# Kernel tuning notes

Hardware: AMD Instinct MI355X
Metric: run time of the kernel (lower is better)

Reference implementation:

```python
import jax, jax.numpy as jnp
import numpy as np

D = 1024        # model dim (== moe_inter_dim, required by Expert's x2*x3)
H = 1024        # expert hidden dim (moe_inter_dim)
E = 8           # n_routed_experts
K = 2           # n_activated_experts (top-k)
I = 2 * 1024    # shared-expert inter dim = n_shared_experts * moe_inter_dim
ROUTE_SCALE = 1.0


def setup_inputs() -> dict:
    key = jax.random.key(0)
    ks = jax.random.split(key, 12)
    s = lambda *sh: 1.0 / np.sqrt(sh[-1])
    return {
        "x":      jax.random.normal(ks[0], (1, 2048, D), jnp.float32),
        "gate_w": jax.random.normal(ks[1], (E, D), jnp.float32) * s(E, D),
        "w1":     jax.random.normal(ks[2], (E, H, D), jnp.float32) * s(H, D),
        "b1":     jax.random.normal(ks[3], (E, H), jnp.float32) * 0.01,
        "w2":     jax.random.normal(ks[4], (E, D, H), jnp.float32) * s(D, H),
        "b2":     jax.random.normal(ks[5], (E, D), jnp.float32) * 0.01,
        "w3":     jax.random.normal(ks[6], (E, H, D), jnp.float32) * s(H, D),
        "b3":     jax.random.normal(ks[7], (E, H), jnp.float32) * 0.01,
        "sw1":    jax.random.normal(ks[8], (I, D), jnp.float32) * s(I, D),
        "sw2":    jax.random.normal(ks[9], (I, D), jnp.float32) * s(I, D),
        "sw3":    jax.random.normal(ks[10], (D, I), jnp.float32) * s(D, I),
    }


def reference(x, gate_w, w1, b1, w2, b2, w3, b3, sw1, sw2, sw3):
    B, S, _ = x.shape
    xt = x.reshape(-1, D)                                  # (T, D)
    # ---- Gate (softmax scoring, n_groups==1, no bias, route_scale=1) ----
    logits = xt @ gate_w.T                                 # (T, E)
    scores = jax.nn.softmax(logits.astype(jnp.float32), axis=-1)
    top_vals, idx = jax.lax.top_k(scores, K)               # (T, K)
    weights = (jnp.take_along_axis(scores, idx, axis=1)
               .astype(x.dtype)) * ROUTE_SCALE             # (T, K)
    # ---- Routed experts: input is scaled by routing weight BEFORE expert ----
    xs = xt[:, None, :] * weights[:, :, None]              # (T, K, D)
    y = jnp.zeros_like(xt)
    for e in range(E):  # fixed small loop over experts (dense masked dispatch)
        mask = (idx == e).astype(x.dtype)                  # (T, K)
        h = jax.nn.silu(jnp.einsum('tkd,hd->tkh', xs, w1[e]) + b1[e])
        x2 = jnp.einsum('tkh,dh->tkd', h, w2[e]) + b2[e]   # (T, K, D)
        x3 = jnp.einsum('tkd,hd->tkh', xs, w3[e]) + b3[e]  # (T, K, H==D)
        y = y + jnp.sum((x2 * x3) * mask[:, :, None], axis=1)
    # ---- Shared experts (SwiGLU MLP, no biases) ----
    z = (jax.nn.silu(xt @ sw1.T) * (xt @ sw2.T)) @ sw3.T   # (T, D)
    return (y + z).reshape(B, S, D)
```

## Files before the change

### kernel.cpp

```cpp
#include <hip/hip_runtime.h>

typedef unsigned short u16;
typedef __attribute__((ext_vector_type(4))) float floatx4;
typedef __attribute__((ext_vector_type(8))) short short8;

#define MAXROWS 5120

__device__ __forceinline__ u16 f2bf(float f) {
    union { float f; unsigned u; } v; v.f = f;
    unsigned r = v.u + 0x7FFF + ((v.u >> 16) & 1);
    return (u16)(r >> 16);
}
__device__ __forceinline__ float bf2f(u16 h) {
    union { unsigned u; float f; } v; v.u = ((unsigned)h) << 16; return v.f;
}
__device__ __forceinline__ float silu_f(float x) { return x / (1.f + __expf(-x)); }

__device__ __forceinline__ void gl_lds16(const void* g, void* l) {
    __builtin_amdgcn_global_load_lds(
        (__attribute__((address_space(1))) unsigned int*)g,
        (__attribute__((address_space(3))) unsigned int*)l, 16, 0, 0);
}

__device__ __forceinline__ void ld_frags(
    unsigned a0, unsigned a1, unsigned a2, unsigned a3,
    unsigned b0, unsigned b1, unsigned b2, unsigned b3,
    short8& af0, short8& af1, short8& af2, short8& af3,
    short8& bf0, short8& bf1, short8& bf2, short8& bf3) {
    asm volatile(
        "ds_read_b128 %0, %8\n\t"
        "ds_read_b128 %1, %9\n\t"
        "ds_read_b128 %2, %10\n\t"
        "ds_read_b128 %3, %11\n\t"
        "ds_read_b128 %4, %12\n\t"
        "ds_read_b128 %5, %13\n\t"
        "ds_read_b128 %6, %14\n\t"
        "ds_read_b128 %7, %15\n\t"
        "s_waitcnt lgkmcnt(0)"
        : "=&v"(af0), "=&v"(af1), "=&v"(af2), "=&v"(af3),
          "=&v"(bf0), "=&v"(bf1), "=&v"(bf2), "=&v"(bf3)
        : "v"(a0), "v"(a1), "v"(a2), "v"(a3),
          "v"(b0), "v"(b1), "v"(b2), "v"(b3));
}

__device__ __forceinline__ void ld_frags4(
    unsigned a0, unsigned a1, unsigned a2, unsigned a3,
    short8& f0, short8& f1, short8& f2, short8& f3) {
    asm volatile(
        "ds_read_b128 %0, %4\n\t"
        "ds_read_b128 %1, %5\n\t"
        "ds_read_b128 %2, %6\n\t"
        "ds_read_b128 %3, %7\n\t"
        "s_waitcnt lgkmcnt(0)"
        : "=&v"(f0), "=&v"(f1), "=&v"(f2), "=&v"(f3)
        : "v"(a0), "v"(a1), "v"(a2), "v"(a3));
}

#define WAIT_VM8() __builtin_amdgcn_s_waitcnt(3960)
#define WAIT_VM4() __builtin_amdgcn_s_waitcnt(3956)
#define WAIT_VM0() __builtin_amdgcn_s_waitcnt(3952)
#define BAR()      __builtin_amdgcn_s_barrier()

__global__ void conv_gate(const float* __restrict__ w1, const float* __restrict__ w2,
                          const float* __restrict__ w3, const float* __restrict__ sw1,
                          const float* __restrict__ sw2, const float* __restrict__ sw3,
                          const float* __restrict__ x, const float* __restrict__ gw,
                          u16* __restrict__ W13, u16* __restrict__ W2b,
                          u16* __restrict__ S12, u16* __restrict__ S3b,
                          u16* __restrict__ Xb,
                          int* __restrict__ idxA, float* __restrict__ wA) {
    int bid = blockIdx.x;
    if (bid < 512) {
        int w = threadIdx.x >> 6, lane = threadIdx.x & 63;
        int t = bid * 4 + w;
        const float* xr = x + (size_t)t * 1024;
        float acc[8];
#pragma unroll
        for (int e = 0; e < 8; e++) acc[e] = 0.f;
#pragma unroll
        for (int i = 0; i < 16; i++) {
            float xv = xr[lane + (i << 6)];
#pragma unroll
            for (int e = 0; e < 8; e++) acc[e] += xv * gw[e * 1024 + lane + (i << 6)];
        }
#pragma unroll
        for (int e = 0; e < 8; e++)
            for (int off = 32; off > 0; off >>= 1) acc[e] += __shfl_xor(acc[e], off);
        if (lane == 0) {
            float m = acc[0];
#pragma unroll
            for (int e = 1; e < 8; e++) m = fmaxf(m, acc[e]);
            float p[8], s = 0.f;
#pragma unroll
            for (int e = 0; e < 8; e++) { p[e] = __expf(acc[e] - m); s += p[e]; }
            float inv = 1.f / s;
#pragma unroll
            for (int e = 0; e < 8; e++) p[e] *= inv;
            int i0 = 0;
#pragma unroll
            for (int e = 1; e < 8; e++) if (p[e] > p[i0]) i0 = e;
            int i1 = (i0 == 0) ? 1 : 0;
            for (int e = i1 + 1; e < 8; e++) if (e != i0 && p[e] > p[i1]) i1 = e;
            idxA[2 * t] = i0; idxA[2 * t + 1] = i1;
            wA[2 * t] = p[i0]; wA[2 * t + 1] = p[i1];
        }
        return;
    }
    long j = (long)(bid - 512) * 256 + threadIdx.x;
    const float* src; u16* dst; long d;
    if (j < 2097152) {
        long e = j >> 18; src = w1; dst = W13; d = j + (e << 18);
    } else if ((j -= 2097152) < 2097152) {
        long e = j >> 18; src = w3; dst = W13; d = j + (e << 18) + 262144;
    } else if ((j -= 2097152) < 2097152) { src = w2;  dst = W2b; d = j; }
    else if ((j -= 2097152) < 524288) {
        long rr = j >> 8, c4 = j & 255;
        long br = ((rr >> 4) << 5) + (rr & 15);
        src = sw1; dst = S12; d = (br << 8) + c4;
    } else if ((j -= 524288) < 524288) {
        long rr = j >> 8, c4 = j & 255;
        long br = ((rr >> 4) << 5) + 16 + (rr & 15);
        src = sw2; dst = S12; d = (br << 8) + c4;
    } else if ((j -= 524288) < 524288)     { src = sw3; dst = S3b; d = j; }
    else { j -= 524288; src = x; dst = Xb; d = j; }
    float4 v = ((const float4*)src)[j];
    ushort4 o; o.x = f2bf(v.x); o.y = f2bf(v.y); o.z = f2bf(v.z); o.w = f2bf(v.w);
    ((ushort4*)dst)[d] = o;
}

__global__ void rank_k(const int* __restrict__ idxA, int* __restrict__ tileexp,
                       int* __restrict__ tilem0, int* __restrict__ tilevalid,
                       int* __restrict__ ntiles, int* __restrict__ slot_of) {
    int lane = threadIdx.x;
    const int* my = idxA + lane * 64;
    int h[8];
#pragma unroll
    for (int e = 0; e < 8; e++) h[e] = 0;
    for (int i = 0; i < 64; i++) {
        int v = my[i];
#pragma unroll
        for (int e = 0; e < 8; e++) h[e] += (v == e);
    }
    int excl[8], tot[8];
#pragma unroll
    for (int e = 0; e < 8; e++) {
        int inc = h[e];
        for (int off = 1; off < 64; off <<= 1) {
            int up = __shfl_up(inc, off);
            if (lane >= off) inc += up;
        }
        excl[e] = inc - h[e];
        tot[e] = __shfl(inc, 63);
    }
    int base[8], tiles = 0;
#pragma unroll
    for (int e = 0; e < 8; e++) {
        base[e] = tiles * 128;
        tiles += (tot[e] + 127) >> 7;
    }
    if (lane == 0) {
        int t256 = 0;
        for (int e = 0; e < 8; e++) {
            int t128 = (tot[e] + 127) >> 7;
            for (int j = 0; j < t128; j += 2) {
                tileexp[t256] = e;
                tilem0[t256] = base[e] + (j << 7);
                tilevalid[t256] = ((t128 - j) >= 2) ? 256 : 128;
                t256++;
            }
        }
        ntiles[0] = t256;
    }
    int c[8];
#pragma unroll
    for (int e = 0; e < 8; e++) c[e] = base[e] + excl[e];
    for (int i = 0; i < 64; i++) {
        int v = my[i], slot = 0;
#pragma unroll
        for (int e = 0; e < 8; e++) slot += (v == e) ? c[e] : 0;
#pragma unroll
        for (int e = 0; e < 8; e++) c[e] += (v == e);
        slot_of[lane * 64 + i] = slot;
    }
}

__global__ void build_xs(const float* __restrict__ x, const float* __restrict__ wA,
                         const int* __restrict__ slot_of, u16* __restrict__ XS) {
    int s = blockIdx.x, i = threadIdx.x;
    int t = s >> 1; float w = wA[s]; int slot = slot_of[s];
    float4 v = ((const float4*)(x + (size_t)t * 1024))[i];
    ushort4 o; o.x = f2bf(v.x * w); o.y = f2bf(v.y * w); o.z = f2bf(v.z * w); o.w = f2bf(v.w * w);
    ((ushort4*)(XS + (size_t)slot * 1024))[i] = o;
}

#define STAGE_PAIR(Ab, Bb, lda, kbeg, TT, RND)                                 \
    {                                                                          \
        int r_ = (w << 4) + ((RND) << 7) + rloc;                               \
        int cg_ = clds ^ ((r_ >> 1) & 3);                                      \
        int kk_ = (kbeg) + ((TT) << 5);                                        \
        int db_ = (((TT) & 3) << 14) + (((w << 4) + ((RND) << 7)) << 5);       \
        gl_lds16((Ab) + (size_t)(m0 + r_) * (lda) + kk_ + (cg_ << 3),          \
                 LDS + db_);                                                   \
        gl_lds16((Bb) + (size_t)(n0 + r_) * (lda) + kk_ + (cg_ << 3),          \
                 LDS + 8192 + db_);                                            \
    }

#define MFMA4(AF, IOFF)                                                        \
    _Pragma("unroll")                                                          \
    for (int i_ = 0; i_ < 4; i_++)                                             \
        _Pragma("unroll")                                                      \
        for (int j_ = 0; j_ < 4; j_++)                                         \
            acc[i_ + (IOFF)][j_] = __builtin_amdgcn_mfma_f32_16x16x32_bf16(    \
                AF[i_], bf[j_], acc[i_ + (IOFF)][j_], 0, 0, 0);

#define KLOOP(NSTEP, Ab, Bb, lda, kbeg)                                        \
    {                                                                          \
        STAGE_PAIR(Ab, Bb, lda, kbeg, 0, 0); STAGE_PAIR(Ab, Bb, lda, kbeg, 0, 1); \
        STAGE_PAIR(Ab, Bb, lda, kbeg, 1, 0); STAGE_PAIR(Ab, Bb, lda, kbeg, 1, 1); \
        STAGE_PAIR(Ab, Bb, lda, kbeg, 2, 0); STAGE_PAIR(Ab, Bb, lda, kbeg, 2, 1); \
        WAIT_VM8(); BAR();                                                     \
        for (int t = 0; t < (NSTEP); t++) {                                    \
            unsigned bo = (unsigned)(t & 3) << 15;                             \
            bool more = (t + 3 < (NSTEP));                                     \
            if (more) STAGE_PAIR(Ab, Bb, lda, kbeg, t + 3, 0);                 \
            short8 af[4], bf[4], a2[4];                                        \
            ld_frags(adA[0] + bo, adA[1] + bo, adA[2] + bo, adA[3] + bo,       \
                     adB[0] + bo, adB[1] + bo, adB[2] + bo, adB[3] + bo,       \
                     af[0], af[1], af[2], af[3], bf[0], bf[1], bf[2], bf[3]);  \
            __builtin_amdgcn_s_setprio(1);                                     \
            MFMA4(af, 0);                                                      \
            __builtin_amdgcn_s_setprio(0);                                     \
            if (more) STAGE_PAIR(Ab, Bb, lda, kbeg, t + 3, 1);                 \
            ld_frags4(adA[4] + bo, adA[5] + bo, adA[6] + bo, adA[7] + bo,      \
                      a2[0], a2[1], a2[2], a2[3]);                             \
            if (t < (NSTEP) - 1) {                                             \
                int rem = (NSTEP) - 1 - t;                                     \
                if (rem >= 3) WAIT_VM8();                                      \
                else if (rem == 2) WAIT_VM4();                                 \
                else WAIT_VM0();                                               \
                BAR();                                                         \
            }                                                                  \
            __builtin_amdgcn_s_setprio(1);                                     \
            MFMA4(a2, 4);                                                      \
            __builtin_amdgcn_s_setprio(0);                                     \
        }                                                                      \
    }

#define GEMM_PRE()                                                             \
    int tid = threadIdx.x, w = tid >> 6, lane = tid & 63;                      \
    int wm = w >> 2, wn = w & 3;                                               \
    int rloc = lane >> 2, clds = lane & 3, q = lane >> 4, l15 = lane & 15;     \
    unsigned ldsbase = (unsigned)(size_t)(__attribute__((address_space(3))) u16*)LDS; \
    unsigned adA[8], adB[4];                                                   \
    _Pragma("unroll")                                                          \
    for (int i = 0; i < 8; i++) {                                              \
        int rr = (wm << 7) + (i << 4) + l15;                                   \
        int g = q ^ ((rr >> 1) & 3);                                           \
        adA[i] = ldsbase + rr * 64 + g * 16;                                   \
    }                                                                          \
    _Pragma("unroll")                                                          \
    for (int j = 0; j < 4; j++) {                                              \
        int rr = (wn << 6) + (j << 4) + l15;                                   \
        int g = q ^ ((rr >> 1) & 3);                                           \
        adB[j] = ldsbase + 16384 + rr * 64 + g * 16;                           \
    }                                                                          \
    floatx4 acc[8][4];                                                         \
    _Pragma("unroll")                                                          \
    for (int i = 0; i < 8; i++)                                                \
        _Pragma("unroll")                                                      \
        for (int j = 0; j < 4; j++) {                                          \
            floatx4 z = {0.f, 0.f, 0.f, 0.f}; acc[i][j] = z;                   \
        }

__global__ __launch_bounds__(512, 2) void gemm_A(
    const u16* __restrict__ XS, const u16* __restrict__ Xb,
    const u16* __restrict__ W13, const u16* __restrict__ S12,
    const float* __restrict__ b1, const float* __restrict__ b3,
    u16* __restrict__ H, u16* __restrict__ X3h, u16* __restrict__ G,
    const int* __restrict__ tileexp, const int* __restrict__ tilem0,
    const int* __restrict__ tilevalid, const int* __restrict__ ntiles) {
    __shared__ u16 LDS[65536];
    int xcd = blockIdx.x & 7, ws = blockIdx.x >> 3;
    const u16 *Ab, *Bb; int m0, n0, nt = 0, e = 0, vcnt = 256; bool routed;
    if (ws < 24) {
        routed = true;
        int mt = xcd * 3 + (ws >> 3);
        nt = ws & 7;
        if (mt >= ntiles[0]) return;
        e = tileexp[mt]; m0 = tilem0[mt]; vcnt = tilevalid[mt];
        n0 = nt * 256;
        Ab = XS; Bb = W13 + ((size_t)e << 21);
    } else {
        routed = false; int s = ws - 24;
        m0 = xcd * 256; n0 = s * 256;
        Ab = Xb; Bb = S12;
    }
    GEMM_PRE();

    KLOOP(32, Ab, Bb, 1024, 0);

    if (routed) {
#pragma unroll
        for (int i = 0; i < 8; i++) {
            if (((wm << 7) + (i << 4)) >= vcnt) continue;
            int rowb = m0 + (wm << 7) + (i << 4) + (q << 2);
#pragma unroll
            for (int j = 0; j < 4; j++) {
                int col = n0 + (wn << 6) + (j << 4) + l15;
#pragma unroll
                for (int r = 0; r < 4; r++) {
                    float v = acc[i][j][r];
                    int rw = rowb + r;
                    if (nt < 4) {
                        H[(size_t)rw * 1024 + col] = f2bf(silu_f(v + b1[e * 1024 + col]));
                    } else {
                        int c2 = col - 1024;
                        X3h[(size_t)rw * 1024 + c2] = f2bf(v + b3[e * 1024 + c2]);
                    }
                }
            }
        }
    } else {
#pragma unroll
        for (int i = 0; i < 8; i++) {
            int rowb = m0 + (wm << 7) + (i << 4) + (q << 2);
#pragma unroll
            for (int jp = 0; jp < 4; jp += 2) {
                int brb = n0 + (wn << 6) + (jp << 4);
                int lcol = ((brb >> 5) << 4) + l15;
#pragma unroll
                for (int r = 0; r < 4; r++) {
                    float u = acc[i][jp][r], v = acc[i][jp + 1][r];
                    G[(size_t)(rowb + r) * 2048 + lcol] = f2bf(silu_f(u) * v);
                }
            }
        }
    }
}

__global__ __launch_bounds__(512, 2) void gemm_B(
    const u16* __restrict__ H, const u16* __restrict__ G,
    const u16* __restrict__ W2b, const u16* __restrict__ S3b,
    const float* __restrict__ b2, const u16* __restrict__ X3h,
    u16* __restrict__ P0, u16* __restrict__ P1, float* __restrict__ Z,
    const int* __restrict__ tileexp, const int* __restrict__ tilem0,
    const int* __restrict__ tilevalid, const int* __restrict__ ntiles) {
    __shared__ u16 LDS[65536];
    int xcd = blockIdx.x & 7, ws = blockIdx.x >> 3;
    const u16 *Ab, *Bb; int m0, n0, kc, kbeg, lda, e = 0, vcnt = 256; bool routed;
    if (ws < 24) {
        routed = true;
        int mt = xcd * 3 + (ws >> 3);
        int r = ws & 7; int nt = r & 3; kc = r >> 2;
        if (mt >= ntiles[0]) return;
        e = tileexp[mt]; m0 = tilem0[mt]; vcnt = tilevalid[mt];
        n0 = nt * 256;
        Ab = H; Bb = W2b + ((size_t)e << 20); lda = 1024; kbeg = kc << 9;
    } else {
        routed = false; int s = ws - 24;
        kc = s >> 2; int nt = s & 3;
        m0 = xcd * 256; n0 = nt * 256;
        Ab = G; Bb = S3b; lda = 2048; kbeg = kc << 9;
    }
    GEMM_PRE();

    KLOOP(16, Ab, Bb, lda, kbeg);

    if (routed) {
        u16* Pk = kc ? P1 : P0;
#pragma unroll
        for (int i = 0; i < 8; i++) {
            if (((wm << 7) + (i << 4)) >= vcnt) continue;
            int rowb = m0 + (wm << 7) + (i << 4) + (q << 2);
#pragma unroll
            for (int j = 0; j < 4; j++) {
                int col = n0 + (wn << 6) + (j << 4) + l15;
#pragma unroll
                for (int r = 0; r < 4; r++) {
                    int rw = rowb + r;
                    float v = acc[i][j][r] + (kc == 0 ? b2[e * 1024 + col] : 0.f);
                    float pv = v * bf2f(X3h[(size_t)rw * 1024 + col]);
                    Pk[(size_t)rw * 1024 + col] = f2bf(pv);
                }
            }
        }
    } else {
        float* Zk = Z + (size_t)kc * 2097152;
#pragma unroll
        for (int i = 0; i < 8; i++) {
            int rowb = m0 + (wm << 7) + (i << 4) + (q << 2);
#pragma unroll
            for (int j = 0; j < 4; j++) {
                int col = n0 + (wn << 6) + (j << 4) + l15;
#pragma unroll
                for (int r = 0; r < 4; r++)
                    Zk[(size_t)(rowb + r) * 1024 + col] = acc[i][j][r];
            }
        }
    }
}

__global__ void final_k(const float* __restrict__ Z,
                        const u16* __restrict__ P0, const u16* __restrict__ P1,
                        const int* __restrict__ slot_of, float* __restrict__ out) {
    int i = blockIdx.x * 256 + threadIdx.x;
    int t = i >> 8, c4 = i & 255;
    int s0 = slot_of[2 * t], s1 = slot_of[2 * t + 1];
    size_t zi = (size_t)t * 256 + c4;
    float4 z0 = ((const float4*)Z)[zi];
    float4 z1 = ((const float4*)(Z + 2097152))[zi];
    float4 z2 = ((const float4*)(Z + 4194304))[zi];
    float4 z3 = ((const float4*)(Z + 6291456))[zi];
    ushort4 a0 = ((const ushort4*)P0)[(size_t)s0 * 256 + c4];
    ushort4 a1 = ((const ushort4*)P1)[(size_t)s0 * 256 + c4];
    ushort4 c0 = ((const ushort4*)P0)[(size_t)s1 * 256 + c4];
    ushort4 c1 = ((const ushort4*)P1)[(size_t)s1 * 256 + c4];
    float4 o;
    o.x = z0.x + z1.x + z2.x + z3.x + bf2f(a0.x) + bf2f(a1.x) + bf2f(c0.x) + bf2f(c1.x);
    o.y = z0.y + z1.y + z2.y + z3.y + bf2f(a0.y) + bf2f(a1.y) + bf2f(c0.y) + bf2f(c1.y);
    o.z = z0.z + z1.z + z2.z + z3.z + bf2f(a0.z) + bf2f(a1.z) + bf2f(c0.z) + bf2f(c1.z);
    o.w = z0.w + z1.w + z2.w + z3.w + bf2f(a0.w) + bf2f(a1.w) + bf2f(c0.w) + bf2f(c1.w);
    ((float4*)out)[(size_t)t * 256 + c4] = o;
}

extern "C" void kernel_launch(void* const* d_in, const int* in_sizes, int n_in,
                              void* d_out, int out_size, void* d_ws, size_t ws_size,
                              hipStream_t stream) {
    const float* x   = (const float*)d_in[0];
    const float* gw  = (const float*)d_in[1];
    const float* w1  = (const float*)d_in[2];
    const float* b1  = (const float*)d_in[3];
    const float* w2  = (const float*)d_in[4];
    const float* b2  = (const float*)d_in[5];
    const float* w3  = (const float*)d_in[6];
    const float* b3  = (const float*)d_in[7];
    const float* sw1 = (const float*)d_in[8];
    const float* sw2 = (const float*)d_in[9];
    const float* sw3 = (const float*)d_in[10];
    float* out = (float*)d_out;

    char* p = (char*)d_ws;
    int* ntiles    = (int*)(p + 192);
    int* tileexp   = (int*)(p + 256);
    int* tilem0    = (int*)(p + 512);
    int* tilevalid = (int*)(p + 768);
    size_t off = 4096;
    u16*   XS      = (u16*)(p + off);   off += (size_t)MAXROWS * 1024 * 2;
    int*   idxA    = (int*)(p + off);   off += 16384;
    float* wA      = (float*)(p + off); off += 16384;
    int*   slot_of = (int*)(p + off);   off += 16384;
    u16*   H       = (u16*)(p + off);   off += (size_t)MAXROWS * 1024 * 2;
    u16*   X3h     = (u16*)(p + off);   off += (size_t)MAXROWS * 1024 * 2;
    u16*   P0      = (u16*)(p + off);   off += (size_t)MAXROWS * 1024 * 2;
    u16*   P1      = (u16*)(p + off);   off += (size_t)MAXROWS * 1024 * 2;
    float* Z       = (float*)(p + off); off += (size_t)4 * 2048 * 1024 * 4;
    u16*   W13     = (u16*)(p + off);   off += (size_t)8 * 2048 * 1024 * 2;
    u16*   W2b     = (u16*)(p + off);   off += (size_t)8 * 1024 * 1024 * 2;
    u16*   S12     = (u16*)(p + off);   off += (size_t)4096 * 1024 * 2;
    u16*   S3b     = (u16*)(p + off);   off += (size_t)1024 * 2048 * 2;
    u16*   Xb      = (u16*)(p + off);   off += (size_t)2048 * 1024 * 2;
    u16*   G       = (u16*)(p + off);   off += (size_t)2048 * 2048 * 2;

    conv_gate<<<33280, 256, 0, stream>>>(w1, w2, w3, sw1, sw2, sw3, x, gw,
                                         W13, W2b, S12, S3b, Xb, idxA, wA);
    rank_k<<<1, 64, 0, stream>>>(idxA, tileexp, tilem0, tilevalid, ntiles, slot_of);
    build_xs<<<4096, 256, 0, stream>>>(x, wA, slot_of, XS);

    gemm_A<<<320, 512, 0, stream>>>(XS, Xb, W13, S12, b1, b3, H, X3h, G,
                                    tileexp, tilem0, tilevalid, ntiles);
    gemm_B<<<320, 512, 0, stream>>>(H, G, W2b, S3b, b2, X3h, P0, P1, Z,
                                    tileexp, tilem0, tilevalid, ntiles);
    final_k<<<2048, 256, 0, stream>>>(Z, P0, P1, slot_of, out);
}
```

Baseline: 309.0 us.

## Software-pipeline LDS fragment loads across k-steps with double-buffered registers

Restructures the GEMM k-loop so the next step's A/B fragments are read from LDS while the current step's MFMAs run. It uses two register sets of fragments, partial lgkmcnt waits, and sched_barriers to keep the compiler from reordering. Launch bounds drop from 2 to 1 waves-per-EU target so the extra live fragment registers fit without spilling. The cost is lower occupancy and more register pressure, and the hand-tuned wait counts add risk of subtle hazards.

```diff
diff --git a/kernel.cpp b/kernel.cpp
--- a/kernel.cpp
+++ b/kernel.cpp
@@ -22,11 +22,25 @@
         (__attribute__((address_space(3))) unsigned int*)l, 16, 0, 0);
 }
 
-__device__ __forceinline__ void ld_frags(
+__device__ __forceinline__ void ds4_waitold(
+    unsigned a0, unsigned a1, unsigned a2, unsigned a3,
+    short8& o0, short8& o1, short8& o2, short8& o3) {
+    asm volatile(
+        "ds_read_b128 %0, %4\n\t"
+        "ds_read_b128 %1, %5\n\t"
+        "ds_read_b128 %2, %6\n\t"
+        "ds_read_b128 %3, %7\n\t"
+        "s_waitcnt lgkmcnt(4)"
+        : "=&v"(o0), "=&v"(o1), "=&v"(o2), "=&v"(o3)
+        : "v"(a0), "v"(a1), "v"(a2), "v"(a3));
+    __builtin_amdgcn_sched_barrier(0);
+}
+
+__device__ __forceinline__ void ds8_waitold(
     unsigned a0, unsigned a1, unsigned a2, unsigned a3,
     unsigned b0, unsigned b1, unsigned b2, unsigned b3,
-    short8& af0, short8& af1, short8& af2, short8& af3,
-    short8& bf0, short8& bf1, short8& bf2, short8& bf3) {
+    short8& o0, short8& o1, short8& o2, short8& o3,
+    short8& o4, short8& o5, short8& o6, short8& o7) {
     asm volatile(
         "ds_read_b128 %0, %8\n\t"
         "ds_read_b128 %1, %9\n\t"
@@ -36,27 +50,16 @@
         "ds_read_b128 %5, %13\n\t"
         "ds_read_b128 %6, %14\n\t"
         "ds_read_b128 %7, %15\n\t"
-        "s_waitcnt lgkmcnt(0)"
-        : "=&v"(af0), "=&v"(af1), "=&v"(af2), "=&v"(af3),
-          "=&v"(bf0), "=&v"(bf1), "=&v"(bf2), "=&v"(bf3)
+        "s_waitcnt lgkmcnt(8)"
+        : "=&v"(o0), "=&v"(o1), "=&v"(o2), "=&v"(o3),
+          "=&v"(o4), "=&v"(o5), "=&v"(o6), "=&v"(o7)
         : "v"(a0), "v"(a1), "v"(a2), "v"(a3),
           "v"(b0), "v"(b1), "v"(b2), "v"(b3));
-}
-
-__device__ __forceinline__ void ld_frags4(
-    unsigned a0, unsigned a1, unsigned a2, unsigned a3,
-    short8& f0, short8& f1, short8& f2, short8& f3) {
-    asm volatile(
-        "ds_read_b128 %0, %4\n\t"
-        "ds_read_b128 %1, %5\n\t"
-        "ds_read_b128 %2, %6\n\t"
-        "ds_read_b128 %3, %7\n\t"
-        "s_waitcnt lgkmcnt(0)"
-        : "=&v"(f0), "=&v"(f1), "=&v"(f2), "=&v"(f3)
-        : "v"(a0), "v"(a1), "v"(a2), "v"(a3));
+    __builtin_amdgcn_sched_barrier(0);
 }
 
 #define WAIT_VM8() __builtin_amdgcn_s_waitcnt(3960)
+#define WAIT_VM6() __builtin_amdgcn_s_waitcnt(3958)
 #define WAIT_VM4() __builtin_amdgcn_s_waitcnt(3956)
 #define WAIT_VM0() __builtin_amdgcn_s_waitcnt(3952)
 #define BAR()      __builtin_amdgcn_s_barrier()
@@ -205,13 +208,44 @@
                  LDS + 8192 + db_);                                            \
     }
 
-#define MFMA4(AF, IOFF)                                                        \
+#define MFMA16(AF, BF, IOFF)                                                   \
+    __builtin_amdgcn_s_setprio(1);                                             \
     _Pragma("unroll")                                                          \
     for (int i_ = 0; i_ < 4; i_++)                                             \
         _Pragma("unroll")                                                      \
         for (int j_ = 0; j_ < 4; j_++)                                         \
             acc[i_ + (IOFF)][j_] = __builtin_amdgcn_mfma_f32_16x16x32_bf16(    \
-                AF[i_], bf[j_], acc[i_ + (IOFF)][j_], 0, 0, 0);
+                (AF)[i_], (BF)[j_], acc[i_ + (IOFF)][j_], 0, 0, 0);            \
+    __builtin_amdgcn_s_setprio(0);                                             \
+    __builtin_amdgcn_sched_barrier(0);
+
+#define KSTEP(T, LOc, Fc, LOn, Fn, NSTEP, Ab, Bb, lda, kbeg)                   \
+    {                                                                          \
+        unsigned bo_ = (unsigned)((T) & 3) << 15;                              \
+        if ((T) + 3 < (NSTEP)) STAGE_PAIR(Ab, Bb, lda, kbeg, (T) + 3, 0);      \
+        short8 ah[4];                                                          \
+        ds4_waitold(adA[4] + bo_, adA[5] + bo_, adA[6] + bo_, adA[7] + bo_,    \
+                    ah[0], ah[1], ah[2], ah[3]);                               \
+        BAR();                                                                 \
+        MFMA16(LOc, Fc, 0);                                                    \
+        if ((T) + 1 < (NSTEP)) {                                               \
+            if ((T) <= (NSTEP) - 4) WAIT_VM6();                                \
+            else if ((T) == (NSTEP) - 3) WAIT_VM4();                           \
+            else WAIT_VM0();                                                   \
+            BAR();                                                             \
+            unsigned bn_ = (unsigned)(((T) + 1) & 3) << 15;                    \
+            ds8_waitold(adA[0] + bn_, adA[1] + bn_, adA[2] + bn_,              \
+                        adA[3] + bn_, adB[0] + bn_, adB[1] + bn_,              \
+                        adB[2] + bn_, adB[3] + bn_,                            \
+                        LOn[0], LOn[1], LOn[2], LOn[3],                        \
+                        Fn[0], Fn[1], Fn[2], Fn[3]);                           \
+            if ((T) + 3 < (NSTEP)) STAGE_PAIR(Ab, Bb, lda, kbeg, (T) + 3, 1);  \
+        } else {                                                               \
+            asm volatile("s_waitcnt lgkmcnt(0)");                              \
+            __builtin_amdgcn_sched_barrier(0);                                 \
+        }                                                                      \
+        MFMA16(ah, Fc, 4);                                                     \
+    }
 
 #define KLOOP(NSTEP, Ab, Bb, lda, kbeg)                                        \
     {                                                                          \
@@ -219,30 +253,14 @@
         STAGE_PAIR(Ab, Bb, lda, kbeg, 1, 0); STAGE_PAIR(Ab, Bb, lda, kbeg, 1, 1); \
         STAGE_PAIR(Ab, Bb, lda, kbeg, 2, 0); STAGE_PAIR(Ab, Bb, lda, kbeg, 2, 1); \
         WAIT_VM8(); BAR();                                                     \
-        for (int t = 0; t < (NSTEP); t++) {                                    \
-            unsigned bo = (unsigned)(t & 3) << 15;                             \
-            bool more = (t + 3 < (NSTEP));                                     \
-            if (more) STAGE_PAIR(Ab, Bb, lda, kbeg, t + 3, 0);                 \
-            short8 af[4], bf[4], a2[4];                                        \
-            ld_frags(adA[0] + bo, adA[1] + bo, adA[2] + bo, adA[3] + bo,       \
-                     adB[0] + bo, adB[1] + bo, adB[2] + bo, adB[3] + bo,       \
-                     af[0], af[1], af[2], af[3], bf[0], bf[1], bf[2], bf[3]);  \
-            __builtin_amdgcn_s_setprio(1);                                     \
-            MFMA4(af, 0);                                                      \
-            __builtin_amdgcn_s_setprio(0);                                     \
-            if (more) STAGE_PAIR(Ab, Bb, lda, kbeg, t + 3, 1);                 \
-            ld_frags4(adA[4] + bo, adA[5] + bo, adA[6] + bo, adA[7] + bo,      \
-                      a2[0], a2[1], a2[2], a2[3]);                             \
-            if (t < (NSTEP) - 1) {                                             \
-                int rem = (NSTEP) - 1 - t;                                     \
-                if (rem >= 3) WAIT_VM8();                                      \
-                else if (rem == 2) WAIT_VM4();                                 \
-                else WAIT_VM0();                                               \
-                BAR();                                                         \
-            }                                                                  \
-            __builtin_amdgcn_s_setprio(1);                                     \
-            MFMA4(a2, 4);                                                      \
-            __builtin_amdgcn_s_setprio(0);                                     \
+        short8 lo0[4], f0[4], lo1[4], f1[4];                                   \
+        ds8_waitold(adA[0], adA[1], adA[2], adA[3],                            \
+                    adB[0], adB[1], adB[2], adB[3],                            \
+                    lo0[0], lo0[1], lo0[2], lo0[3],                            \
+                    f0[0], f0[1], f0[2], f0[3]);                               \
+        for (int t = 0; t < (NSTEP); t += 2) {                                 \
+            KSTEP(t,     lo0, f0, lo1, f1, NSTEP, Ab, Bb, lda, kbeg);          \
+            KSTEP(t + 1, lo1, f1, lo0, f0, NSTEP, Ab, Bb, lda, kbeg);          \
         }                                                                      \
     }
 
@@ -272,7 +290,7 @@
             floatx4 z = {0.f, 0.f, 0.f, 0.f}; acc[i][j] = z;                   \
         }
 
-__global__ __launch_bounds__(512, 2) void gemm_A(
+__global__ __launch_bounds__(512, 1) void gemm_A(
     const u16* __restrict__ XS, const u16* __restrict__ Xb,
     const u16* __restrict__ W13, const u16* __restrict__ S12,
     const float* __restrict__ b1, const float* __restrict__ b3,
@@ -338,7 +356,7 @@
     }
 }
 
-__global__ __launch_bounds__(512, 2) void gemm_B(
+__global__ __launch_bounds__(512, 1) void gemm_B(
     const u16* __restrict__ H, const u16* __restrict__ G,
     const u16* __restrict__ W2b, const u16* __restrict__ S3b,
     const float* __restrict__ b2, const u16* __restrict__ X3h,
```

Result: no change. 314.1 us (+1.6%).

## Shrink GEMM tiles to 256x128 with triple-buffered LDS pipeline and more blocks

Applied to the files above, without the earlier changes.

Both MoE GEMM kernels move from 256x256 output tiles with a 4-deep LDS ring to 256x128 tiles with a 3-buffer ring. LDS use drops to about 72KB and launch bounds rise to 4 blocks per SM. The grid grows from 320 to 896 blocks and the XCD-aware block mapping is removed, which aims at better occupancy and load balance. The cost is lower per-block arithmetic intensity, an extra barrier per k-step, and the loss of the L2 locality the XCD mapping gave. rank_k also preloads its 64 indices per lane with vector loads and fully unrolls its loops.

```diff
diff --git a/kernel.cpp b/kernel.cpp
--- a/kernel.cpp
+++ b/kernel.cpp
@@ -43,21 +43,8 @@
           "v"(b0), "v"(b1), "v"(b2), "v"(b3));
 }
 
-__device__ __forceinline__ void ld_frags4(
-    unsigned a0, unsigned a1, unsigned a2, unsigned a3,
-    short8& f0, short8& f1, short8& f2, short8& f3) {
-    asm volatile(
-        "ds_read_b128 %0, %4\n\t"
-        "ds_read_b128 %1, %5\n\t"
-        "ds_read_b128 %2, %6\n\t"
-        "ds_read_b128 %3, %7\n\t"
-        "s_waitcnt lgkmcnt(0)"
-        : "=&v"(f0), "=&v"(f1), "=&v"(f2), "=&v"(f3)
-        : "v"(a0), "v"(a1), "v"(a2), "v"(a3));
-}
-
-#define WAIT_VM8() __builtin_amdgcn_s_waitcnt(3960)
-#define WAIT_VM4() __builtin_amdgcn_s_waitcnt(3956)
+#define WAIT_VM6() __builtin_amdgcn_s_waitcnt(3958)
+#define WAIT_VM3() __builtin_amdgcn_s_waitcnt(3955)
 #define WAIT_VM0() __builtin_amdgcn_s_waitcnt(3952)
 #define BAR()      __builtin_amdgcn_s_barrier()
 
@@ -132,14 +119,21 @@
                        int* __restrict__ tilem0, int* __restrict__ tilevalid,
                        int* __restrict__ ntiles, int* __restrict__ slot_of) {
     int lane = threadIdx.x;
-    const int* my = idxA + lane * 64;
+    const int4* my4 = (const int4*)(idxA + lane * 64);
+    int v[64];
+#pragma unroll
+    for (int k = 0; k < 16; k++) {
+        int4 t4 = my4[k];
+        v[4 * k] = t4.x; v[4 * k + 1] = t4.y; v[4 * k + 2] = t4.z; v[4 * k + 3] = t4.w;
+    }
     int h[8];
 #pragma unroll
     for (int e = 0; e < 8; e++) h[e] = 0;
+#pragma unroll
     for (int i = 0; i < 64; i++) {
-        int v = my[i];
-#pragma unroll
-        for (int e = 0; e < 8; e++) h[e] += (v == e);
+        int t = v[i];
+#pragma unroll
+        for (int e = 0; e < 8; e++) h[e] += (t == e);
     }
     int excl[8], tot[8];
 #pragma unroll
@@ -174,13 +168,15 @@
     int c[8];
 #pragma unroll
     for (int e = 0; e < 8; e++) c[e] = base[e] + excl[e];
+    int* so = slot_of + lane * 64;
+#pragma unroll
     for (int i = 0; i < 64; i++) {
-        int v = my[i], slot = 0;
-#pragma unroll
-        for (int e = 0; e < 8; e++) slot += (v == e) ? c[e] : 0;
-#pragma unroll
-        for (int e = 0; e < 8; e++) c[e] += (v == e);
-        slot_of[lane * 64 + i] = slot;
+        int t = v[i], slot = 0;
+#pragma unroll
+        for (int e = 0; e < 8; e++) slot += (t == e) ? c[e] : 0;
+#pragma unroll
+        for (int e = 0; e < 8; e++) c[e] += (t == e);
+        so[i] = slot;
     }
 }
 
@@ -193,68 +189,65 @@
     ((ushort4*)(XS + (size_t)slot * 1024))[i] = o;
 }
 
-#define STAGE_PAIR(Ab, Bb, lda, kbeg, TT, RND)                                 \
+#define STAGE3(BUF, Ab, Bb, lda, kk)                                           \
     {                                                                          \
-        int r_ = (w << 4) + ((RND) << 7) + rloc;                               \
-        int cg_ = clds ^ ((r_ >> 1) & 3);                                      \
-        int kk_ = (kbeg) + ((TT) << 5);                                        \
-        int db_ = (((TT) & 3) << 14) + (((w << 4) + ((RND) << 7)) << 5);       \
-        gl_lds16((Ab) + (size_t)(m0 + r_) * (lda) + kk_ + (cg_ << 3),          \
-                 LDS + db_);                                                   \
-        gl_lds16((Bb) + (size_t)(n0 + r_) * (lda) + kk_ + (cg_ << 3),          \
-                 LDS + 8192 + db_);                                            \
-    }
-
-#define MFMA4(AF, IOFF)                                                        \
-    _Pragma("unroll")                                                          \
-    for (int i_ = 0; i_ < 4; i_++)                                             \
+        int rA_ = (w << 4) + rloc;                                             \
+        int cgA_ = clds ^ ((rA_ >> 1) & 3);                                    \
+        gl_lds16((Ab) + (size_t)(m0 + rA_) * (lda) + (kk) + (cgA_ << 3),       \
+                 LDS + (BUF) * 12288 + (w << 9));                              \
+        int rA2_ = rA_ + 128;                                                  \
+        int cgA2_ = clds ^ ((rA2_ >> 1) & 3);                                  \
+        gl_lds16((Ab) + (size_t)(m0 + rA2_) * (lda) + (kk) + (cgA2_ << 3),     \
+                 LDS + (BUF) * 12288 + (w << 9) + 4096);                       \
+        gl_lds16((Bb) + (size_t)(n0 + rA_) * (lda) + (kk) + (cgA_ << 3),       \
+                 LDS + (BUF) * 12288 + 8192 + (w << 9));                       \
+    }
+
+#define COMPUTE(BUF)                                                           \
+    {                                                                          \
+        unsigned bo = (unsigned)(BUF) * 24576u;                                \
+        short8 af[4], bf[4];                                                   \
+        ld_frags(adA[0] + bo, adA[1] + bo, adA[2] + bo, adA[3] + bo,           \
+                 adB[0] + bo, adB[1] + bo, adB[2] + bo, adB[3] + bo,           \
+                 af[0], af[1], af[2], af[3], bf[0], bf[1], bf[2], bf[3]);      \
+        __builtin_amdgcn_s_setprio(1);                                         \
         _Pragma("unroll")                                                      \
-        for (int j_ = 0; j_ < 4; j_++)                                         \
-            acc[i_ + (IOFF)][j_] = __builtin_amdgcn_mfma_f32_16x16x32_bf16(    \
-                AF[i_], bf[j_], acc[i_ + (IOFF)][j_], 0, 0, 0);
+        for (int i_ = 0; i_ < 4; i_++)                                         \
+            _Pragma("unroll")                                                  \
+            for (int j_ = 0; j_ < 4; j_++)                                     \
+                acc[i_][j_] = __builtin_amdgcn_mfma_f32_16x16x32_bf16(         \
+                    af[i_], bf[j_], acc[i_][j_], 0, 0, 0);                     \
+        __builtin_amdgcn_s_setprio(0);                                         \
+    }
 
 #define KLOOP(NSTEP, Ab, Bb, lda, kbeg)                                        \
     {                                                                          \
-        STAGE_PAIR(Ab, Bb, lda, kbeg, 0, 0); STAGE_PAIR(Ab, Bb, lda, kbeg, 0, 1); \
-        STAGE_PAIR(Ab, Bb, lda, kbeg, 1, 0); STAGE_PAIR(Ab, Bb, lda, kbeg, 1, 1); \
-        STAGE_PAIR(Ab, Bb, lda, kbeg, 2, 0); STAGE_PAIR(Ab, Bb, lda, kbeg, 2, 1); \
-        WAIT_VM8(); BAR();                                                     \
+        STAGE3(0, Ab, Bb, lda, (kbeg));                                        \
+        STAGE3(1, Ab, Bb, lda, (kbeg) + 32);                                   \
         for (int t = 0; t < (NSTEP); t++) {                                    \
-            unsigned bo = (unsigned)(t & 3) << 15;                             \
-            bool more = (t + 3 < (NSTEP));                                     \
-            if (more) STAGE_PAIR(Ab, Bb, lda, kbeg, t + 3, 0);                 \
-            short8 af[4], bf[4], a2[4];                                        \
-            ld_frags(adA[0] + bo, adA[1] + bo, adA[2] + bo, adA[3] + bo,       \
-                     adB[0] + bo, adB[1] + bo, adB[2] + bo, adB[3] + bo,       \
-                     af[0], af[1], af[2], af[3], bf[0], bf[1], bf[2], bf[3]);  \
-            __builtin_amdgcn_s_setprio(1);                                     \
-            MFMA4(af, 0);                                                      \
-            __builtin_amdgcn_s_setprio(0);                                     \
-            if (more) STAGE_PAIR(Ab, Bb, lda, kbeg, t + 3, 1);                 \
-            ld_frags4(adA[4] + bo, adA[5] + bo, adA[6] + bo, adA[7] + bo,      \
-                      a2[0], a2[1], a2[2], a2[3]);                             \
-            if (t < (NSTEP) - 1) {                                             \
-                int rem = (NSTEP) - 1 - t;                                     \
-                if (rem >= 3) WAIT_VM8();                                      \
-                else if (rem == 2) WAIT_VM4();                                 \
-                else WAIT_VM0();                                               \
-                BAR();                                                         \
+            if (t + 2 < (NSTEP)) {                                             \
+                STAGE3((t + 2) % 3, Ab, Bb, lda, (kbeg) + ((t + 2) << 5));     \
+                WAIT_VM6();                                                    \
+            } else if (t + 1 < (NSTEP)) {                                      \
+                WAIT_VM3();                                                    \
+            } else {                                                           \
+                WAIT_VM0();                                                    \
             }                                                                  \
-            __builtin_amdgcn_s_setprio(1);                                     \
-            MFMA4(a2, 4);                                                      \
-            __builtin_amdgcn_s_setprio(0);                                     \
+            BAR();                                                             \
+            COMPUTE(t % 3);                                                    \
+            BAR();                                                             \
         }                                                                      \
     }
 
 #define GEMM_PRE()                                                             \
     int tid = threadIdx.x, w = tid >> 6, lane = tid & 63;                      \
-    int wm = w >> 2, wn = w & 3;                                               \
+    int wm = w >> 1, wn = w & 1;                                               \
     int rloc = lane >> 2, clds = lane & 3, q = lane >> 4, l15 = lane & 15;     \
     unsigned ldsbase = (unsigned)(size_t)(__attribute__((address_space(3))) u16*)LDS; \
-    unsigned adA[8], adB[4];                                                   \
+    unsigned adA[4], adB[4];                                                   \
     _Pragma("unroll")                                                          \
-    for (int i = 0; i < 8; i++) {                                              \
-        int rr = (wm << 7) + (i << 4) + l15;                                   \
+    for (int i = 0; i < 4; i++) {                                              \
+        int rr = (wm << 6) + (i << 4) + l15;                                   \
         int g = q ^ ((rr >> 1) & 3);                                           \
         adA[i] = ldsbase + rr * 64 + g * 16;                                   \
     }                                                                          \
@@ -264,35 +257,35 @@
         int g = q ^ ((rr >> 1) & 3);                                           \
         adB[j] = ldsbase + 16384 + rr * 64 + g * 16;                           \
     }                                                                          \
-    floatx4 acc[8][4];                                                         \
+    floatx4 acc[4][4];                                                         \
     _Pragma("unroll")                                                          \
-    for (int i = 0; i < 8; i++)                                                \
+    for (int i = 0; i < 4; i++)                                                \
         _Pragma("unroll")                                                      \
         for (int j = 0; j < 4; j++) {                                          \
             floatx4 z = {0.f, 0.f, 0.f, 0.f}; acc[i][j] = z;                   \
         }
 
-__global__ __launch_bounds__(512, 2) void gemm_A(
+__global__ __launch_bounds__(512, 4) void gemm_A(
     const u16* __restrict__ XS, const u16* __restrict__ Xb,
     const u16* __restrict__ W13, const u16* __restrict__ S12,
     const float* __restrict__ b1, const float* __restrict__ b3,
     u16* __restrict__ H, u16* __restrict__ X3h, u16* __restrict__ G,
     const int* __restrict__ tileexp, const int* __restrict__ tilem0,
     const int* __restrict__ tilevalid, const int* __restrict__ ntiles) {
-    __shared__ u16 LDS[65536];
-    int xcd = blockIdx.x & 7, ws = blockIdx.x >> 3;
+    __shared__ u16 LDS[36864];
+    int bid = blockIdx.x;
     const u16 *Ab, *Bb; int m0, n0, nt = 0, e = 0, vcnt = 256; bool routed;
-    if (ws < 24) {
+    if (bid < 640) {
         routed = true;
-        int mt = xcd * 3 + (ws >> 3);
-        nt = ws & 7;
+        int mt = bid >> 4;
+        nt = bid & 15;
         if (mt >= ntiles[0]) return;
         e = tileexp[mt]; m0 = tilem0[mt]; vcnt = tilevalid[mt];
-        n0 = nt * 256;
+        n0 = nt << 7;
         Ab = XS; Bb = W13 + ((size_t)e << 21);
     } else {
-        routed = false; int s = ws - 24;
-        m0 = xcd * 256; n0 = s * 256;
+        routed = false; int s = bid - 640;
+        m0 = (s >> 5) << 8; n0 = (s & 31) << 7;
         Ab = Xb; Bb = S12;
     }
     GEMM_PRE();
@@ -301,9 +294,9 @@
 
     if (routed) {
 #pragma unroll
-        for (int i = 0; i < 8; i++) {
-            if (((wm << 7) + (i << 4)) >= vcnt) continue;
-            int rowb = m0 + (wm << 7) + (i << 4) + (q << 2);
+        for (int i = 0; i < 4; i++) {
+            if (((wm << 6) + (i << 4)) >= vcnt) continue;
+            int rowb = m0 + (wm << 6) + (i << 4) + (q << 2);
 #pragma unroll
             for (int j = 0; j < 4; j++) {
                 int col = n0 + (wn << 6) + (j << 4) + l15;
@@ -311,7 +304,7 @@
                 for (int r = 0; r < 4; r++) {
                     float v = acc[i][j][r];
                     int rw = rowb + r;
-                    if (nt < 4) {
+                    if (nt < 8) {
                         H[(size_t)rw * 1024 + col] = f2bf(silu_f(v + b1[e * 1024 + col]));
                     } else {
                         int c2 = col - 1024;
@@ -322,8 +315,8 @@
         }
     } else {
 #pragma unroll
-        for (int i = 0; i < 8; i++) {
-            int rowb = m0 + (wm << 7) + (i << 4) + (q << 2);
+        for (int i = 0; i < 4; i++) {
+            int rowb = m0 + (wm << 6) + (i << 4) + (q << 2);
 #pragma unroll
             for (int jp = 0; jp < 4; jp += 2) {
                 int brb = n0 + (wn << 6) + (jp << 4);
@@ -338,28 +331,27 @@
     }
 }
 
-__global__ __launch_bounds__(512, 2) void gemm_B(
+__global__ __launch_bounds__(512, 4) void gemm_B(
     const u16* __restrict__ H, const u16* __restrict__ G,
     const u16* __restrict__ W2b, const u16* __restrict__ S3b,
     const float* __restrict__ b2, const u16* __restrict__ X3h,
     u16* __restrict__ P0, u16* __restrict__ P1, float* __restrict__ Z,
     const int* __restrict__ tileexp, const int* __restrict__ tilem0,
     const int* __restrict__ tilevalid, const int* __restrict__ ntiles) {
-    __shared__ u16 LDS[65536];
-    int xcd = blockIdx.x & 7, ws = blockIdx.x >> 3;
+    __shared__ u16 LDS[36864];
+    int bid = blockIdx.x;
     const u16 *Ab, *Bb; int m0, n0, kc, kbeg, lda, e = 0, vcnt = 256; bool routed;
-    if (ws < 24) {
+    if (bid < 640) {
         routed = true;
-        int mt = xcd * 3 + (ws >> 3);
-        int r = ws & 7; int nt = r & 3; kc = r >> 2;
+        int mt = bid >> 4;
+        int r = bid & 15; int nt = r & 7; kc = r >> 3;
         if (mt >= ntiles[0]) return;
         e = tileexp[mt]; m0 = tilem0[mt]; vcnt = tilevalid[mt];
-        n0 = nt * 256;
+        n0 = nt << 7;
         Ab = H; Bb = W2b + ((size_t)e << 20); lda = 1024; kbeg = kc << 9;
     } else {
-        routed = false; int s = ws - 24;
-        kc = s >> 2; int nt = s & 3;
-        m0 = xcd * 256; n0 = nt * 256;
+        routed = false; int s = bid - 640;
+        m0 = (s >> 5) << 8; n0 = ((s & 31) >> 2) << 7; kc = s & 3;
         Ab = G; Bb = S3b; lda = 2048; kbeg = kc << 9;
     }
     GEMM_PRE();
@@ -369,9 +361,9 @@
     if (routed) {
         u16* Pk = kc ? P1 : P0;
 #pragma unroll
-        for (int i = 0; i < 8; i++) {
-            if (((wm << 7) + (i << 4)) >= vcnt) continue;
-            int rowb = m0 + (wm << 7) + (i << 4) + (q << 2);
+        for (int i = 0; i < 4; i++) {
+            if (((wm << 6) + (i << 4)) >= vcnt) continue;
+            int rowb = m0 + (wm << 6) + (i << 4) + (q << 2);
 #pragma unroll
             for (int j = 0; j < 4; j++) {
                 int col = n0 + (wn << 6) + (j << 4) + l15;
@@ -387,8 +379,8 @@
     } else {
         float* Zk = Z + (size_t)kc * 2097152;
 #pragma unroll
-        for (int i = 0; i < 8; i++) {
-            int rowb = m0 + (wm << 7) + (i << 4) + (q << 2);
+        for (int i = 0; i < 4; i++) {
+            int rowb = m0 + (wm << 6) + (i << 4) + (q << 2);
 #pragma unroll
             for (int j = 0; j < 4; j++) {
                 int col = n0 + (wn << 6) + (j << 4) + l15;
@@ -466,9 +458,9 @@
     rank_k<<<1, 64, 0, stream>>>(idxA, tileexp, tilem0, tilevalid, ntiles, slot_of);
     build_xs<<<4096, 256, 0, stream>>>(x, wA, slot_of, XS);
 
-    gemm_A<<<320, 512, 0, stream>>>(XS, Xb, W13, S12, b1, b3, H, X3h, G,
+    gemm_A<<<896, 512, 0, stream>>>(XS, Xb, W13, S12, b1, b3, H, X3h, G,
                                     tileexp, tilem0, tilevalid, ntiles);
-    gemm_B<<<320, 512, 0, stream>>>(H, G, W2b, S3b, b2, X3h, P0, P1, Z,
+    gemm_B<<<896, 512, 0, stream>>>(H, G, W2b, S3b, b2, X3h, P0, P1, Z,
                                     tileexp, tilem0, tilevalid, ntiles);
     final_k<<<2048, 256, 0, stream>>>(Z, P0, P1, slot_of, out);
 }
```

Result: slower. 448.4 us (+45.1%).
